# Kernel tuning notes

Hardware: AMD Instinct MI355X
Metric: run time of the kernel (lower is better)

## Reference

```python
import jax, jax.numpy as jnp
import numpy as np

B, T, D, H = 2, 2048, 2048, 32
HD = D // H
# quantization scales (constructor-time attributes in the original repo)
A_PROJ = 3e-4   # q/k/v proj alpha (W8A8B8O8Linear)
A_QK = 2e-5     # qk_bmm alpha (BMM_S8T_S8N_F32T)
A_PV = 1e-2     # pv_bmm alpha (BMM_S8T_S8N_S8T)
A_OUT = 1e-4    # out_proj alpha (W8A8BFP32OFP32Linear)


def _i8(key, shape):
    return jax.random.randint(key, shape, -128, 128, dtype=jnp.int32).astype(jnp.int8)


def setup_inputs() -> dict:
    key = jax.random.key(0)
    ks = jax.random.split(key, 10)
    hidden_states = _i8(ks[0], (B, T, D))
    # causal mask, 0 on/below diagonal, large negative above
    causal = jnp.triu(jnp.full((T, T), -1e9, dtype=jnp.float32), k=1)
    attention_mask = jnp.broadcast_to(causal, (B, 1, T, T))
    return {
        "hidden_states": hidden_states,
        "attention_mask": attention_mask,
        "Wq": _i8(ks[1], (D, D)), "bq": _i8(ks[2], (D,)),
        "Wk": _i8(ks[3], (D, D)), "bk": _i8(ks[4], (D,)),
        "Wv": _i8(ks[5], (D, D)), "bv": _i8(ks[6], (D,)),
        "Wo": _i8(ks[7], (D, D)),
        "bo": jax.random.normal(ks[8], (D,), dtype=jnp.float32),
    }


def _w8a8b8o8(x_i8, W_i8, b_i8, alpha):
    # int8 GEMM -> int32 accum; epilogue: alpha*acc + bias, saturate to int8
    acc = jnp.einsum('btk,nk->btn', x_i8.astype(jnp.int32), W_i8.astype(jnp.int32))
    y = alpha * acc.astype(jnp.float32) + b_i8.astype(jnp.float32)
    return jnp.clip(jnp.round(y), -128, 127).astype(jnp.int8)


def reference(hidden_states, attention_mask, Wq, bq, Wk, bk, Wv, bv, Wo, bo):
    # q/k/v projections: int8 in, int8 out
    q = _w8a8b8o8(hidden_states, Wq, bq, A_PROJ)
    k = _w8a8b8o8(hidden_states, Wk, bk, A_PROJ)
    v = _w8a8b8o8(hidden_states, Wv, bv, A_PROJ)

    def shape(x):  # [B,T,D] -> [B,H,T,HD]
        return x.reshape(B, T, H, HD).transpose(0, 2, 1, 3)

    qh, kh, vh = shape(q), shape(k), shape(v)

    # qk_bmm (BMM_S8T_S8N_F32T): fp32 = alpha * int8 q @ k^T
    attn = A_QK * jnp.einsum('bhtd,bhsd->bhts',
                             qh.astype(jnp.int32), kh.astype(jnp.int32)).astype(jnp.float32)
    attn = attn + attention_mask  # [B,1,T,T] broadcasts over heads
    attn = jnp.maximum(attn, jnp.finfo(jnp.float32).min)
    probs = jax.nn.softmax(attn, axis=-1)

    # quantize probs: p.mul_(127).round_() -> int8
    p_i8 = jnp.clip(jnp.round(probs * 127.0), -128, 127).astype(jnp.int8)

    # pv_bmm (BMM_S8T_S8N_S8T): int8 out = sat(round(alpha * p @ v))
    pv = jnp.einsum('bhts,bhsd->bhtd', p_i8.astype(jnp.int32), vh.astype(jnp.int32))
    attn_out_i8 = jnp.clip(jnp.round(A_PV * pv.astype(jnp.float32)), -128, 127).astype(jnp.int8)

    # [B,H,T,HD] -> [B,T,D]
    attn_out = attn_out_i8.transpose(0, 2, 1, 3).reshape(B, T, D)

    # out_proj (W8A8BFP32OFP32Linear): fp32 = alpha*(x@W^T) + fp32 bias
    acc = jnp.einsum('btk,nk->btn', attn_out.astype(jnp.int32), Wo.astype(jnp.int32))
    out = A_OUT * acc.astype(jnp.float32) + bo
    return out
```

## Files before the change

kernel.cpp:

```cpp
#include <hip/hip_runtime.h>
#include <cstdint>

#define A_PROJ 3e-4f
#define A_QK   2e-5f
#define A_PV   1e-2f
#define A_OUT  1e-4f

#define NB 2
#define NT 2048
#define ND 2048
#define NH 32
#define NHD 64
#define NM (NB*NT)

typedef int v4i __attribute__((ext_vector_type(4)));

__device__ __forceinline__ int8_t sat8(float y) {
  float r = rintf(y);
  r = fminf(fmaxf(r, -128.f), 127.f);
  return (int8_t)(int)r;
}

__device__ __forceinline__ float exp2_fast(float x) {
  return __builtin_amdgcn_exp2f(x);
}

__device__ __forceinline__ void gl2lds16(const int8_t* g, int8_t* l) {
  __builtin_amdgcn_global_load_lds(
      (const __attribute__((address_space(1))) void*)g,
      (__attribute__((address_space(3))) void*)l, 16, 0, 0);
}

__device__ __forceinline__ uint32_t pack_lo4(float f0, float f1, float f2, float f3) {
  uint32_t u0 = __float_as_uint(f0), u1 = __float_as_uint(f1);
  uint32_t u2 = __float_as_uint(f2), u3 = __float_as_uint(f3);
  uint32_t lo = __builtin_amdgcn_perm(u1, u0, 0x04000400u);
  uint32_t hi = __builtin_amdgcn_perm(u3, u2, 0x04000400u);
  return __builtin_amdgcn_perm(hi, lo, 0x05040100u);
}

#define NWW (ND*ND/4)
__global__ void pack_all(const int* __restrict__ X,
                         const int* __restrict__ W0, const int* __restrict__ W1,
                         const int* __restrict__ W2, const int* __restrict__ W3,
                         int8_t* __restrict__ dX, int8_t* __restrict__ dW0,
                         int8_t* __restrict__ dW1, int8_t* __restrict__ dW2,
                         int8_t* __restrict__ dW3) {
  int i = blockIdx.x * blockDim.x + threadIdx.x;
  const int nx = NM*ND/4;
  const int* src; int8_t* dst; int off;
  if (i < nx) { src = X; dst = dX; off = i; }
  else {
    int j = i - nx;
    int r = j >> 20;
    off = j & (NWW - 1);
    src = (r == 0) ? W0 : (r == 1) ? W1 : (r == 2) ? W2 : W3;
    dst = (r == 0) ? dW0 : (r == 1) ? dW1 : (r == 2) ? dW2 : dW3;
  }
  int4 v = ((const int4*)src)[off];
  uint32_t p = (uint32_t)(v.x & 255) | ((uint32_t)(v.y & 255) << 8) |
               ((uint32_t)(v.z & 255) << 16) | ((uint32_t)(v.w & 255) << 24);
  ((uint32_t*)dst)[off] = p;
}

__global__ __launch_bounds__(256) void gemm_qkv(
    const int8_t* __restrict__ X,
    const int8_t* __restrict__ Wq, const int8_t* __restrict__ Wk, const int8_t* __restrict__ Wv,
    const int* __restrict__ bq, const int* __restrict__ bk, const int* __restrict__ bv,
    int8_t* __restrict__ Qh, int8_t* __restrict__ Kh, int8_t* __restrict__ Vt)
{
  __shared__ __align__(16) int8_t As[2][128][64];
  __shared__ __align__(16) int8_t Bs[2][128][64];
  const int z = blockIdx.z;
  const int8_t* W  = (z == 0) ? Wq : ((z == 1) ? Wk : Wv);
  const int* bias  = (z == 0) ? bq : ((z == 1) ? bk : bv);
  const int m0 = blockIdx.x * 128, n0 = blockIdx.y * 128;
  const int tid = threadIdx.x, lane = tid & 63, wave = tid >> 6;
  const int wm = wave >> 1, wn = wave & 1;
  const int l15 = lane & 15, quad = lane >> 4;

  const int srow = lane >> 2;
  const int scol = (((lane & 3) ^ ((lane >> 3) & 3)) * 16);
  const int rqcol = (quad ^ ((l15 >> 1) & 3)) * 16;

  v4i acc[4][4];
  const v4i vzero = {0, 0, 0, 0};
  #pragma unroll
  for (int i = 0; i < 4; ++i)
    #pragma unroll
    for (int j = 0; j < 4; ++j) acc[i][j] = vzero;

  for (int k0 = 0; k0 < ND; k0 += 128) {
    #pragma unroll
    for (int j = 0; j < 8; ++j) {
      int slot = j * 4 + wave;
      int sl = slot & 15;
      int hh = sl >> 3, rblk = sl & 7;
      int row = rblk * 16 + srow;
      if (slot < 16) {
        gl2lds16(&X[(size_t)(m0 + row) * ND + k0 + hh * 64 + scol], &As[hh][rblk * 16][0]);
      } else {
        gl2lds16(&W[(size_t)(n0 + row) * ND + k0 + hh * 64 + scol], &Bs[hh][rblk * 16][0]);
      }
    }
    __syncthreads();
    #pragma unroll
    for (int hh = 0; hh < 2; ++hh) {
      v4i a[4], b[4];
      #pragma unroll
      for (int mt = 0; mt < 4; ++mt) a[mt] = *(const v4i*)&As[hh][wm*64 + mt*16 + l15][rqcol];
      #pragma unroll
      for (int nt = 0; nt < 4; ++nt) b[nt] = *(const v4i*)&Bs[hh][wn*64 + nt*16 + l15][rqcol];
      #pragma unroll
      for (int mt = 0; mt < 4; ++mt)
        #pragma unroll
        for (int nt = 0; nt < 4; ++nt)
          acc[mt][nt] = __builtin_amdgcn_mfma_i32_16x16x64_i8(a[mt], b[nt], acc[mt][nt], 0, 0, 0);
    }
    __syncthreads();
  }

  float bf[4];
  #pragma unroll
  for (int nt = 0; nt < 4; ++nt) bf[nt] = (float)bias[n0 + wn*64 + nt*16 + l15];

  if (z == 2) {
    #pragma unroll
    for (int mt = 0; mt < 4; ++mt)
      #pragma unroll
      for (int nt = 0; nt < 4; ++nt) {
        int tbase = (m0 + wm*64 + mt*16 + quad*4) & (NT - 1);
        int bb = (m0 + wm*64) >> 11;
        int n = n0 + wn*64 + nt*16 + l15;
        int hh = n >> 6, hd = n & (NHD - 1);
        uint32_t pk = 0;
        #pragma unroll
        for (int r = 0; r < 4; ++r) {
          uint32_t q = (uint32_t)(uint8_t)sat8(A_PROJ * (float)acc[mt][nt][r] + bf[nt]);
          pk |= q << (8 * r);
        }
        size_t bh = (size_t)bb * NH + hh;
        *(uint32_t*)&Vt[(bh * NHD + hd) * NT + tbase] = pk;
      }
  } else {
    int8_t* O = (z == 0) ? Qh : Kh;
    #pragma unroll
    for (int mt = 0; mt < 4; ++mt)
      #pragma unroll
      for (int nt = 0; nt < 4; ++nt)
        #pragma unroll
        for (int r = 0; r < 4; ++r) {
          int m = m0 + wm*64 + mt*16 + quad*4 + r;
          int n = n0 + wn*64 + nt*16 + l15;
          int8_t q = sat8(A_PROJ * (float)acc[mt][nt][r] + bf[nt]);
          int bb = m >> 11, t = m & (NT - 1);
          int hh = n >> 6, hd = n & (NHD - 1);
          size_t bh = (size_t)bb * NH + hh;
          O[(bh * NT + t) * NHD + hd] = q;
        }
  }
}

__global__ __launch_bounds__(256) void attn_fused(
    const int8_t* __restrict__ Qh, const int8_t* __restrict__ Kh, const int8_t* __restrict__ Vt,
    int8_t* __restrict__ AO)
{
  __shared__ __align__(16) int8_t Ks[128][64];
  __shared__ __align__(16) int8_t Vs[64][128];
  __shared__ __align__(16) uint32_t Ps32[4][16][36];

  const int xq = blockIdx.x;
  const int bh = blockIdx.y;
  const int tid = threadIdx.x, lane = tid & 63, wave = tid >> 6;
  const int l15 = lane & 15, quad = lane >> 4;
  const v4i vzero = {0, 0, 0, 0};
  const float MAGIC = 12582912.0f;
  const float C2 = 2.8853900817779268e-05f;

  const int8_t* Qp = Qh + (size_t)bh * NT * NHD;
  const int8_t* Kp = Kh + (size_t)bh * NT * NHD;
  const int8_t* Vp = Vt + (size_t)bh * NHD * NT;
  const int bb = bh >> 5, hhead = bh & (NH - 1);

  const int kst_row = lane >> 2;
  const int kst_col = (((lane & 3) ^ ((lane >> 3) & 3)) * 16);
  const int vst_row = lane >> 3;
  const int vst_col = (((lane & 7) ^ ((lane >> 3) & 7)) * 16);
  const int kfcol = (quad ^ ((l15 >> 1) & 3)) * 16;

  const int t0 = xq * 64;
  const int sd = xq >> 1;
  const int tme = t0 + wave * 16 + l15;

  v4i qf = *(const v4i*)&Qp[(size_t)(t0 + wave * 16 + l15) * NHD + quad * 16];

  float lsum = 0.f;
  for (int st = 0; st <= sd; ++st) {
    const int s0 = st * 128;
    #pragma unroll
    for (int j = 0; j < 2; ++j)
      gl2lds16(&Kp[(size_t)(s0 + j*64 + wave*16 + kst_row) * NHD + kst_col],
               &Ks[j*64 + wave*16][0]);
    __syncthreads();
    v4i kf[8];
    #pragma unroll
    for (int mt = 0; mt < 8; ++mt) kf[mt] = *(const v4i*)&Ks[mt*16 + l15][kfcol];
    if (st < sd) {
      #pragma unroll
      for (int mt = 0; mt < 8; ++mt) {
        v4i sa = __builtin_amdgcn_mfma_i32_16x16x64_i8(kf[mt], qf, vzero, 0, 0, 0);
        #pragma unroll
        for (int r = 0; r < 4; ++r) lsum += exp2_fast(C2 * (float)sa[r]);
      }
    } else {
      #pragma unroll
      for (int mt = 0; mt < 8; ++mt) {
        v4i sa = __builtin_amdgcn_mfma_i32_16x16x64_i8(kf[mt], qf, vzero, 0, 0, 0);
        const int sbase = s0 + mt*16 + quad*4;
        #pragma unroll
        for (int r = 0; r < 4; ++r) {
          float e = exp2_fast(C2 * (float)sa[r]);
          lsum += (sbase + r <= tme) ? e : 0.f;
        }
      }
    }
    __syncthreads();
  }
  {
    lsum += __shfl_xor(lsum, 16, 64);
    lsum += __shfl_xor(lsum, 32, 64);
  }
  const float linv = 127.0f / lsum;

  v4i accv[4];
  #pragma unroll
  for (int j = 0; j < 4; ++j) accv[j] = vzero;

  for (int st = 0; st <= sd; ++st) {
    const int s0 = st * 128;
    #pragma unroll
    for (int j = 0; j < 2; ++j)
      gl2lds16(&Kp[(size_t)(s0 + j*64 + wave*16 + kst_row) * NHD + kst_col],
               &Ks[j*64 + wave*16][0]);
    #pragma unroll
    for (int j = 0; j < 2; ++j)
      gl2lds16(&Vp[(size_t)(j*32 + wave*8 + vst_row) * NT + s0 + vst_col],
               &Vs[j*32 + wave*8][0]);
    __syncthreads();
    v4i kf[8];
    #pragma unroll
    for (int mt = 0; mt < 8; ++mt) kf[mt] = *(const v4i*)&Ks[mt*16 + l15][kfcol];

    if (st < sd) {
      #pragma unroll
      for (int mt = 0; mt < 8; ++mt) {
        v4i sa = __builtin_amdgcn_mfma_i32_16x16x64_i8(kf[mt], qf, vzero, 0, 0, 0);
        float f[4];
        #pragma unroll
        for (int r = 0; r < 4; ++r) {
          float e = exp2_fast(C2 * (float)sa[r]);
          f[r] = fmaf(e, linv, MAGIC);
        }
        Ps32[wave][l15][mt*4 + quad] = pack_lo4(f[0], f[1], f[2], f[3]);
      }
    } else {
      #pragma unroll
      for (int mt = 0; mt < 8; ++mt) {
        v4i sa = __builtin_amdgcn_mfma_i32_16x16x64_i8(kf[mt], qf, vzero, 0, 0, 0);
        const int sbase = s0 + mt*16 + quad*4;
        float f[4];
        #pragma unroll
        for (int r = 0; r < 4; ++r) {
          float e = (sbase + r <= tme) ? exp2_fast(C2 * (float)sa[r]) : 0.f;
          f[r] = fmaf(e, linv, MAGIC);
        }
        Ps32[wave][l15][mt*4 + quad] = pack_lo4(f[0], f[1], f[2], f[3]);
      }
    }
    #pragma unroll
    for (int ks = 0; ks < 2; ++ks) {
      v4i ap = *(const v4i*)&Ps32[wave][l15][ks*16 + quad*4];
      #pragma unroll
      for (int nt2 = 0; nt2 < 4; ++nt2) {
        v4i bv = *(const v4i*)&Vs[nt2*16 + l15][(((ks*4 + quad) ^ (l15 & 7)) * 16)];
        accv[nt2] = __builtin_amdgcn_mfma_i32_16x16x64_i8(ap, bv, accv[nt2], 0, 0, 0);
      }
    }
    __syncthreads();
  }

  #pragma unroll
  for (int nt2 = 0; nt2 < 4; ++nt2)
    #pragma unroll
    for (int r = 0; r < 4; ++r) {
      int t = t0 + wave*16 + quad*4 + r;
      int d = nt2*16 + l15;
      AO[((size_t)bb * NT + t) * ND + hhead * NHD + d] = sat8(A_PV * (float)accv[nt2][r]);
    }
}

__global__ __launch_bounds__(256) void gemm_out(
    const int8_t* __restrict__ X, const int8_t* __restrict__ W,
    const float* __restrict__ bo, float* __restrict__ out)
{
  __shared__ __align__(16) int8_t As[2][128][64];
  __shared__ __align__(16) int8_t Bs[2][128][64];
  const int m0 = blockIdx.x * 128, n0 = blockIdx.y * 128;
  const int tid = threadIdx.x, lane = tid & 63, wave = tid >> 6;
  const int wm = wave >> 1, wn = wave & 1;
  const int l15 = lane & 15, quad = lane >> 4;
  const int srow = lane >> 2;
  const int scol = (((lane & 3) ^ ((lane >> 3) & 3)) * 16);
  const int rqcol = (quad ^ ((l15 >> 1) & 3)) * 16;

  v4i acc[4][4];
  const v4i vzero = {0, 0, 0, 0};
  #pragma unroll
  for (int i = 0; i < 4; ++i)
    #pragma unroll
    for (int j = 0; j < 4; ++j) acc[i][j] = vzero;

  for (int k0 = 0; k0 < ND; k0 += 128) {
    #pragma unroll
    for (int j = 0; j < 8; ++j) {
      int slot = j * 4 + wave;
      int sl = slot & 15;
      int hh = sl >> 3, rblk = sl & 7;
      int row = rblk * 16 + srow;
      if (slot < 16) {
        gl2lds16(&X[(size_t)(m0 + row) * ND + k0 + hh * 64 + scol], &As[hh][rblk * 16][0]);
      } else {
        gl2lds16(&W[(size_t)(n0 + row) * ND + k0 + hh * 64 + scol], &Bs[hh][rblk * 16][0]);
      }
    }
    __syncthreads();
    #pragma unroll
    for (int hh = 0; hh < 2; ++hh) {
      v4i a[4], b[4];
      #pragma unroll
      for (int mt = 0; mt < 4; ++mt) a[mt] = *(const v4i*)&As[hh][wm*64 + mt*16 + l15][rqcol];
      #pragma unroll
      for (int nt = 0; nt < 4; ++nt) b[nt] = *(const v4i*)&Bs[hh][wn*64 + nt*16 + l15][rqcol];
      #pragma unroll
      for (int mt = 0; mt < 4; ++mt)
        #pragma unroll
        for (int nt = 0; nt < 4; ++nt)
          acc[mt][nt] = __builtin_amdgcn_mfma_i32_16x16x64_i8(a[mt], b[nt], acc[mt][nt], 0, 0, 0);
    }
    __syncthreads();
  }

  float bf[4];
  #pragma unroll
  for (int nt = 0; nt < 4; ++nt) bf[nt] = bo[n0 + wn*64 + nt*16 + l15];

  #pragma unroll
  for (int mt = 0; mt < 4; ++mt)
    #pragma unroll
    for (int nt = 0; nt < 4; ++nt)
      #pragma unroll
      for (int r = 0; r < 4; ++r) {
        int m = m0 + wm*64 + mt*16 + quad*4 + r;
        int n = n0 + wn*64 + nt*16 + l15;
        out[(size_t)m * ND + n] = A_OUT * (float)acc[mt][nt][r] + bf[nt];
      }
}

extern "C" void kernel_launch(void* const* d_in, const int* in_sizes, int n_in,
                              void* d_out, int out_size, void* d_ws, size_t ws_size,
                              hipStream_t stream)
{
  const int*   hs  = (const int*)d_in[0];
  const int*   Wq  = (const int*)d_in[2];
  const int*   bq  = (const int*)d_in[3];
  const int*   Wk  = (const int*)d_in[4];
  const int*   bkb = (const int*)d_in[5];
  const int*   Wv  = (const int*)d_in[6];
  const int*   bvb = (const int*)d_in[7];
  const int*   Wo  = (const int*)d_in[8];
  const float* bo  = (const float*)d_in[9];
  float* out = (float*)d_out;

  char* ws = (char*)d_ws;
  const size_t SZ_X = (size_t)NM * ND;
  const size_t SZ_W = (size_t)ND * ND;
  const size_t SZ_H = (size_t)NB * NH * NT * NHD;
  int8_t* Xp  = (int8_t*)ws;
  int8_t* Wqp = (int8_t*)(ws + SZ_X);
  int8_t* Wkp = Wqp + SZ_W;
  int8_t* Wvp = Wkp + SZ_W;
  int8_t* Wop = Wvp + SZ_W;
  int8_t* Qh  = Wop + SZ_W;
  int8_t* Kh  = Qh + SZ_H;
  int8_t* Vt  = Kh + SZ_H;
  int8_t* AO  = Xp;

  const int ntot = (int)(SZ_X/4 + 4 * (SZ_W/4));
  pack_all<<<(ntot + 255) / 256, 256, 0, stream>>>(hs, Wq, Wk, Wv, Wo,
                                                   Xp, Wqp, Wkp, Wvp, Wop);

  gemm_qkv<<<dim3(NM/128, ND/128, 3), 256, 0, stream>>>(Xp, Wqp, Wkp, Wvp, bq, bkb, bvb, Qh, Kh, Vt);
  attn_fused<<<dim3(32, NB*NH), 256, 0, stream>>>(Qh, Kh, Vt, AO);
  gemm_out<<<dim3(NM/128, ND/128), 256, 0, stream>>>(AO, Wop, bo, out);
}
```

Measured before the change: 367.6 us.

## Pair causal query tiles per block and split key tiles across two wave groups

Each attention block now handles two query tiles (bx and 31-bx) so causal work is balanced across blocks, and uses 512 threads. The two groups of four waves each take half of every 128-key tile, then combine softmax sums and PV accumulators through shared memory. This targets load imbalance from the causal triangle and shortens each wave's serial chain, at the cost of extra syncs and cross-group reductions.

```diff
diff --git a/kernel.cpp b/kernel.cpp
--- a/kernel.cpp
+++ b/kernel.cpp
@@ -161,17 +161,19 @@
   }
 }
 
-__global__ __launch_bounds__(256) void attn_fused(
+__global__ __launch_bounds__(512, 8) void attn_fused(
     const int8_t* __restrict__ Qh, const int8_t* __restrict__ Kh, const int8_t* __restrict__ Vt,
     int8_t* __restrict__ AO)
 {
   __shared__ __align__(16) int8_t Ks[128][64];
   __shared__ __align__(16) int8_t Vs[64][128];
-  __shared__ __align__(16) uint32_t Ps32[4][16][36];
-
-  const int xq = blockIdx.x;
+  __shared__ __align__(16) uint32_t Ps32[8][16][20];
+  __shared__ float Lsh[2][4][16];
+
+  const int bx = blockIdx.x;
   const int bh = blockIdx.y;
   const int tid = threadIdx.x, lane = tid & 63, wave = tid >> 6;
+  const int wlocal = wave & 3, group = wave >> 2;
   const int l15 = lane & 15, quad = lane >> 4;
   const v4i vzero = {0, 0, 0, 0};
   const float MAGIC = 12582912.0f;
@@ -187,116 +189,129 @@
   const int vst_row = lane >> 3;
   const int vst_col = (((lane & 7) ^ ((lane >> 3) & 7)) * 16);
   const int kfcol = (quad ^ ((l15 >> 1) & 3)) * 16;
-
-  const int t0 = xq * 64;
-  const int sd = xq >> 1;
-  const int tme = t0 + wave * 16 + l15;
-
-  v4i qf = *(const v4i*)&Qp[(size_t)(t0 + wave * 16 + l15) * NHD + quad * 16];
-
-  float lsum = 0.f;
-  for (int st = 0; st <= sd; ++st) {
-    const int s0 = st * 128;
-    #pragma unroll
-    for (int j = 0; j < 2; ++j)
-      gl2lds16(&Kp[(size_t)(s0 + j*64 + wave*16 + kst_row) * NHD + kst_col],
-               &Ks[j*64 + wave*16][0]);
-    __syncthreads();
-    v4i kf[8];
-    #pragma unroll
-    for (int mt = 0; mt < 8; ++mt) kf[mt] = *(const v4i*)&Ks[mt*16 + l15][kfcol];
-    if (st < sd) {
-      #pragma unroll
-      for (int mt = 0; mt < 8; ++mt) {
-        v4i sa = __builtin_amdgcn_mfma_i32_16x16x64_i8(kf[mt], qf, vzero, 0, 0, 0);
-        #pragma unroll
-        for (int r = 0; r < 4; ++r) lsum += exp2_fast(C2 * (float)sa[r]);
-      }
-    } else {
-      #pragma unroll
-      for (int mt = 0; mt < 8; ++mt) {
-        v4i sa = __builtin_amdgcn_mfma_i32_16x16x64_i8(kf[mt], qf, vzero, 0, 0, 0);
-        const int sbase = s0 + mt*16 + quad*4;
-        #pragma unroll
-        for (int r = 0; r < 4; ++r) {
-          float e = exp2_fast(C2 * (float)sa[r]);
-          lsum += (sbase + r <= tme) ? e : 0.f;
-        }
-      }
-    }
-    __syncthreads();
-  }
-  {
+  const int soff = group * 64;
+
+  for (int half = 0; half < 2; ++half) {
+    const int xq = half ? (31 - bx) : bx;
+    const int t0 = xq * 64;
+    const int sd = xq >> 1;
+    const int tme = t0 + wlocal * 16 + l15;
+    const bool gmask = (group == (xq & 1));
+    const bool gskip = (group == 1) && !(xq & 1);
+
+    v4i qf = *(const v4i*)&Qp[(size_t)(t0 + wlocal * 16 + l15) * NHD + quad * 16];
+
+    float lsum = 0.f;
+    for (int st = 0; st <= sd; ++st) {
+      const int s0 = st * 128;
+      gl2lds16(&Kp[(size_t)(s0 + wave*16 + kst_row) * NHD + kst_col], &Ks[wave*16][0]);
+      __syncthreads();
+      if (!(st == sd && gskip)) {
+        v4i kf[4];
+        #pragma unroll
+        for (int mt = 0; mt < 4; ++mt) kf[mt] = *(const v4i*)&Ks[soff + mt*16 + l15][kfcol];
+        if (st == sd && gmask) {
+          #pragma unroll
+          for (int mt = 0; mt < 4; ++mt) {
+            v4i sa = __builtin_amdgcn_mfma_i32_16x16x64_i8(kf[mt], qf, vzero, 0, 0, 0);
+            const int sbase = s0 + soff + mt*16 + quad*4;
+            #pragma unroll
+            for (int r = 0; r < 4; ++r) {
+              float e = exp2_fast(C2 * (float)sa[r]);
+              lsum += (sbase + r <= tme) ? e : 0.f;
+            }
+          }
+        } else {
+          #pragma unroll
+          for (int mt = 0; mt < 4; ++mt) {
+            v4i sa = __builtin_amdgcn_mfma_i32_16x16x64_i8(kf[mt], qf, vzero, 0, 0, 0);
+            #pragma unroll
+            for (int r = 0; r < 4; ++r) lsum += exp2_fast(C2 * (float)sa[r]);
+          }
+        }
+      }
+      __syncthreads();
+    }
     lsum += __shfl_xor(lsum, 16, 64);
     lsum += __shfl_xor(lsum, 32, 64);
+    if (quad == 0) Lsh[group][wlocal][l15] = lsum;
+    __syncthreads();
+    lsum += Lsh[group ^ 1][wlocal][l15];
+    const float linv = 127.0f / lsum;
+
+    v4i accv[4];
+    #pragma unroll
+    for (int j = 0; j < 4; ++j) accv[j] = vzero;
+
+    for (int st = 0; st <= sd; ++st) {
+      const int s0 = st * 128;
+      gl2lds16(&Kp[(size_t)(s0 + wave*16 + kst_row) * NHD + kst_col], &Ks[wave*16][0]);
+      gl2lds16(&Vp[(size_t)(wave*8 + vst_row) * NT + s0 + vst_col], &Vs[wave*8][0]);
+      __syncthreads();
+      if (!(st == sd && gskip)) {
+        v4i kf[4];
+        #pragma unroll
+        for (int mt = 0; mt < 4; ++mt) kf[mt] = *(const v4i*)&Ks[soff + mt*16 + l15][kfcol];
+
+        if (st == sd && gmask) {
+          #pragma unroll
+          for (int mt = 0; mt < 4; ++mt) {
+            v4i sa = __builtin_amdgcn_mfma_i32_16x16x64_i8(kf[mt], qf, vzero, 0, 0, 0);
+            const int sbase = s0 + soff + mt*16 + quad*4;
+            float f[4];
+            #pragma unroll
+            for (int r = 0; r < 4; ++r) {
+              float e = (sbase + r <= tme) ? exp2_fast(C2 * (float)sa[r]) : 0.f;
+              f[r] = fmaf(e, linv, MAGIC);
+            }
+            Ps32[wave][l15][mt*4 + quad] = pack_lo4(f[0], f[1], f[2], f[3]);
+          }
+        } else {
+          #pragma unroll
+          for (int mt = 0; mt < 4; ++mt) {
+            v4i sa = __builtin_amdgcn_mfma_i32_16x16x64_i8(kf[mt], qf, vzero, 0, 0, 0);
+            float f[4];
+            #pragma unroll
+            for (int r = 0; r < 4; ++r) {
+              float e = exp2_fast(C2 * (float)sa[r]);
+              f[r] = fmaf(e, linv, MAGIC);
+            }
+            Ps32[wave][l15][mt*4 + quad] = pack_lo4(f[0], f[1], f[2], f[3]);
+          }
+        }
+        v4i ap = *(const v4i*)&Ps32[wave][l15][quad*4];
+        #pragma unroll
+        for (int nt2 = 0; nt2 < 4; ++nt2) {
+          v4i bv = *(const v4i*)&Vs[nt2*16 + l15][(((group*4 + quad) ^ (l15 & 7)) * 16)];
+          accv[nt2] = __builtin_amdgcn_mfma_i32_16x16x64_i8(ap, bv, accv[nt2], 0, 0, 0);
+        }
+      }
+      __syncthreads();
+    }
+
+    v4i* AccA = (v4i*)&Ks[0][0];
+    v4i* AccB = (v4i*)&Vs[0][0];
+    const int cbase = (wlocal * 64 + lane) * 2;
+    if (group == 1) {
+      AccA[cbase + 0] = accv[0];  AccA[cbase + 1] = accv[1];
+      AccB[cbase + 0] = accv[2];  AccB[cbase + 1] = accv[3];
+    }
+    __syncthreads();
+    if (group == 0) {
+      v4i p0 = AccA[cbase + 0], p1 = AccA[cbase + 1];
+      v4i p2 = AccB[cbase + 0], p3 = AccB[cbase + 1];
+      accv[0] += p0;  accv[1] += p1;  accv[2] += p2;  accv[3] += p3;
+      #pragma unroll
+      for (int nt2 = 0; nt2 < 4; ++nt2)
+        #pragma unroll
+        for (int r = 0; r < 4; ++r) {
+          int t = t0 + wlocal*16 + quad*4 + r;
+          int d = nt2*16 + l15;
+          AO[((size_t)bb * NT + t) * ND + hhead * NHD + d] = sat8(A_PV * (float)accv[nt2][r]);
+        }
+    }
+    __syncthreads();
   }
-  const float linv = 127.0f / lsum;
-
-  v4i accv[4];
-  #pragma unroll
-  for (int j = 0; j < 4; ++j) accv[j] = vzero;
-
-  for (int st = 0; st <= sd; ++st) {
-    const int s0 = st * 128;
-    #pragma unroll
-    for (int j = 0; j < 2; ++j)
-      gl2lds16(&Kp[(size_t)(s0 + j*64 + wave*16 + kst_row) * NHD + kst_col],
-               &Ks[j*64 + wave*16][0]);
-    #pragma unroll
-    for (int j = 0; j < 2; ++j)
-      gl2lds16(&Vp[(size_t)(j*32 + wave*8 + vst_row) * NT + s0 + vst_col],
-               &Vs[j*32 + wave*8][0]);
-    __syncthreads();
-    v4i kf[8];
-    #pragma unroll
-    for (int mt = 0; mt < 8; ++mt) kf[mt] = *(const v4i*)&Ks[mt*16 + l15][kfcol];
-
-    if (st < sd) {
-      #pragma unroll
-      for (int mt = 0; mt < 8; ++mt) {
-        v4i sa = __builtin_amdgcn_mfma_i32_16x16x64_i8(kf[mt], qf, vzero, 0, 0, 0);
-        float f[4];
-        #pragma unroll
-        for (int r = 0; r < 4; ++r) {
-          float e = exp2_fast(C2 * (float)sa[r]);
-          f[r] = fmaf(e, linv, MAGIC);
-        }
-        Ps32[wave][l15][mt*4 + quad] = pack_lo4(f[0], f[1], f[2], f[3]);
-      }
-    } else {
-      #pragma unroll
-      for (int mt = 0; mt < 8; ++mt) {
-        v4i sa = __builtin_amdgcn_mfma_i32_16x16x64_i8(kf[mt], qf, vzero, 0, 0, 0);
-        const int sbase = s0 + mt*16 + quad*4;
-        float f[4];
-        #pragma unroll
-        for (int r = 0; r < 4; ++r) {
-          float e = (sbase + r <= tme) ? exp2_fast(C2 * (float)sa[r]) : 0.f;
-          f[r] = fmaf(e, linv, MAGIC);
-        }
-        Ps32[wave][l15][mt*4 + quad] = pack_lo4(f[0], f[1], f[2], f[3]);
-      }
-    }
-    #pragma unroll
-    for (int ks = 0; ks < 2; ++ks) {
-      v4i ap = *(const v4i*)&Ps32[wave][l15][ks*16 + quad*4];
-      #pragma unroll
-      for (int nt2 = 0; nt2 < 4; ++nt2) {
-        v4i bv = *(const v4i*)&Vs[nt2*16 + l15][(((ks*4 + quad) ^ (l15 & 7)) * 16)];
-        accv[nt2] = __builtin_amdgcn_mfma_i32_16x16x64_i8(ap, bv, accv[nt2], 0, 0, 0);
-      }
-    }
-    __syncthreads();
-  }
-
-  #pragma unroll
-  for (int nt2 = 0; nt2 < 4; ++nt2)
-    #pragma unroll
-    for (int r = 0; r < 4; ++r) {
-      int t = t0 + wave*16 + quad*4 + r;
-      int d = nt2*16 + l15;
-      AO[((size_t)bb * NT + t) * ND + hhead * NHD + d] = sat8(A_PV * (float)accv[nt2][r]);
-    }
 }
 
 __global__ __launch_bounds__(256) void gemm_out(
@@ -400,6 +415,6 @@
                                                    Xp, Wqp, Wkp, Wvp, Wop);
 
   gemm_qkv<<<dim3(NM/128, ND/128, 3), 256, 0, stream>>>(Xp, Wqp, Wkp, Wvp, bq, bkb, bvb, Qh, Kh, Vt);
-  attn_fused<<<dim3(32, NB*NH), 256, 0, stream>>>(Qh, Kh, Vt, AO);
+  attn_fused<<<dim3(16, NB*NH), 512, 0, stream>>>(Qh, Kh, Vt, AO);
   gemm_out<<<dim3(NM/128, ND/128), 256, 0, stream>>>(AO, Wop, bo, out);
 }
```

Result: faster. 325.2 us (-11.5%).
